# Kernel tuning notes

Hardware: AMD Instinct MI355X
Metric: run time of the kernel (lower is better)

Reference implementation:

```python
import jax, jax.numpy as jnp
import numpy as np

B, T, I, H, O = 128, 512, 512, 2048, 512  # batch, seq_length, input, hidden, output


def setup_inputs() -> dict:
    key = jax.random.key(0)
    ks = jax.random.split(key, 8)
    s_ih = 1.0 / np.sqrt(H)  # torch RNNCell/Linear default init scale 1/sqrt(hidden)
    body = jax.random.normal(ks[0], (B, T - 1, I), dtype=jnp.float32)
    # last timestep row stores the integer pad index (as float), per the module's protocol
    pad = jax.random.randint(ks[1], (B,), 0, T - 2)
    last = jnp.broadcast_to(pad[:, None, None].astype(jnp.float32), (B, 1, I))
    x = jnp.concatenate([body, last], axis=1)  # [B, T, I]
    W_ih = jax.random.uniform(ks[2], (H, I), jnp.float32, -s_ih, s_ih)
    W_hh = jax.random.uniform(ks[3], (H, H), jnp.float32, -s_ih, s_ih)
    b_ih = jax.random.uniform(ks[4], (H,), jnp.float32, -s_ih, s_ih)
    b_hh = jax.random.uniform(ks[5], (H,), jnp.float32, -s_ih, s_ih)
    W_fc = jax.random.uniform(ks[6], (O, H), jnp.float32, -s_ih, s_ih)
    b_fc = jax.random.uniform(ks[7], (O,), jnp.float32, -s_ih, s_ih)
    h0 = jnp.ones((H,), jnp.float32)  # self.h parameter, ones-initialized
    return {"x": x, "h0": h0, "W_ih": W_ih, "b_ih": b_ih, "W_hh": W_hh,
            "b_hh": b_hh, "W_fc": W_fc, "b_fc": b_fc}


def reference(x, h0, W_ih, b_ih, W_hh, b_hh, W_fc, b_fc):
    steps = T - 2  # loop runs over x.shape[2]-1 = (T-1)-1 timesteps
    pad = x[:, -1, 0].astype(jnp.int32)          # [B] pad indices
    xs = jnp.transpose(x[:, :steps, :], (1, 0, 2))  # [steps, B, I]
    h_init = jnp.broadcast_to(h0, (x.shape[0], H))  # self.h * ones([B,1])

    def step(h, xt):
        h = jnp.tanh(xt @ W_ih.T + b_ih + h @ W_hh.T + b_hh)
        return h, h @ W_fc.T + b_fc

    _, outs = jax.lax.scan(step, h_init, xs)     # [steps, B, O]
    # mask selects the single timestep j == pad_len[b]; everything else is zeroed
    mask = (pad[None, :] == jnp.arange(steps)[:, None]).astype(outs.dtype)  # [steps, B]
    return jnp.sum(outs * mask[:, :, None], axis=0)  # [B, O]
```

## Files before the change

kernel.cpp:

```cpp
#include <hip/hip_runtime.h>

#define Bsz 128
#define Tsz 512
#define Isz 512
#define Hsz 2048
#define Osz 512
#define STEPS 510

typedef short short8 __attribute__((ext_vector_type(8)));
typedef float floatx4 __attribute__((ext_vector_type(4)));

__device__ __forceinline__ unsigned short f2bf(float f) {
  unsigned int u = __builtin_bit_cast(unsigned int, f);
  u += 0x7FFFu + ((u >> 16) & 1u);
  return (unsigned short)(u >> 16);
}

template <int AUX>
__device__ __forceinline__ void gload_lds16(const void* g, void* l) {
  __builtin_amdgcn_global_load_lds(
      (const __attribute__((address_space(1))) void*)g,
      (__attribute__((address_space(3))) void*)l, 16, 0, AUX);
}

#define HSTR 2056
#define XSTR 520
#define XBUF (16 * XSTR)

__global__ __launch_bounds__(256, 1)
void rnn_kernel(const float* __restrict__ x, const float* __restrict__ h0v,
                const float* __restrict__ W_ih, const float* __restrict__ b_ih,
                const float* __restrict__ W_hh, const float* __restrict__ b_hh,
                unsigned short* __restrict__ hbuf,
                float* __restrict__ hfinal,
                unsigned int* __restrict__ flags)
{
  __shared__ short h_lds[16 * HSTR];
  __shared__ short x_lds[2 * XBUF];
  __shared__ float red_lds[4 * 16 * 64];
  __shared__ int pad_lds[16];

  const int tid = threadIdx.x;
  const int lane = tid & 63;
  const int wv = tid >> 6;
  const int m16 = lane & 15;
  const int quad = lane >> 4;
  const int rg = blockIdx.x & 7;
  const int cg = blockIdx.x >> 3;
  const int b0 = rg * 16;
  const int c0 = cg * 64;
  const int kq = wv * 512;
  const int kqx = wv * 128;

  short8 wf[16][4];
  short8 wih[4][4];
#pragma unroll
  for (int nt = 0; nt < 4; ++nt) {
    const int wrow = c0 + nt * 16 + m16;
    const float* base = W_hh + (size_t)wrow * Hsz + kq + quad * 8;
#pragma unroll
    for (int kc = 0; kc < 16; ++kc) {
      short8 v;
#pragma unroll
      for (int j = 0; j < 8; ++j) v[j] = (short)f2bf(base[kc * 32 + j]);
      wf[kc][nt] = v;
    }
    const float* basex = W_ih + (size_t)wrow * Isz + kqx + quad * 8;
#pragma unroll
    for (int kc = 0; kc < 4; ++kc) {
      short8 v;
#pragma unroll
      for (int j = 0; j < 8; ++j) v[j] = (short)f2bf(basex[kc * 32 + j]);
      wih[kc][nt] = v;
    }
  }

  const int rrow = tid >> 4;
  const int rcb = (tid & 15) * 4;
  float bias[4];
#pragma unroll
  for (int i = 0; i < 4; ++i) bias[i] = b_ih[c0 + rcb + i] + b_hh[c0 + rcb + i];

  if (tid < 16)
    pad_lds[tid] = (int)x[(size_t)(b0 + tid) * (Tsz * Isz) + (size_t)(Tsz - 1) * Isz];

  for (int k = tid; k < Hsz; k += 256) {
    const short v = (short)f2bf(h0v[k]);
#pragma unroll
    for (int r = 0; r < 16; ++r) h_lds[r * HSTR + k] = v;
  }

  {
    const float* xp = x + (size_t)(b0 + rrow) * (Tsz * Isz);
    short* xb = x_lds + rrow * XSTR;
#pragma unroll
    for (int it = 0; it < 8; ++it) {
      const int i0 = it * 64 + (tid & 15) * 4;
      const float4 v = *reinterpret_cast<const float4*>(xp + i0);
      unsigned long long pk = (unsigned long long)f2bf(v.x) |
                              ((unsigned long long)f2bf(v.y) << 16) |
                              ((unsigned long long)f2bf(v.z) << 32) |
                              ((unsigned long long)f2bf(v.w) << 48);
      *reinterpret_cast<unsigned long long*>(xb + i0) = pk;
    }
  }

  unsigned int* myflag = flags + rg * 32;

  for (int t = 0; t < STEPS; ++t) {
    const bool have_next = (t + 1) < STEPS;

    float4 xv[8];
    if (have_next) {
      const float* xp = x + (size_t)(b0 + rrow) * (Tsz * Isz) + (size_t)(t + 1) * Isz;
#pragma unroll
      for (int it = 0; it < 8; ++it)
        xv[it] = *reinterpret_cast<const float4*>(xp + it * 64 + (tid & 15) * 4);
    }

    if (t > 0) {
      if (tid == 0) {
        const unsigned int target = (unsigned int)(32 * t);
        while (__hip_atomic_load(myflag, __ATOMIC_RELAXED, __HIP_MEMORY_SCOPE_AGENT) < target)
          __builtin_amdgcn_s_sleep(2);
      }
      __syncthreads();
      const unsigned short* hsrc = hbuf + (size_t)(t & 1) * (Bsz * Hsz);
#pragma unroll
      for (int r2 = 0; r2 < 4; ++r2) {
        const int row = wv * 4 + r2;
#pragma unroll
        for (int ch = 0; ch < 4; ++ch) {
          gload_lds16<0x11>(hsrc + (size_t)(b0 + row) * Hsz + ch * 512 + lane * 8,
                            &h_lds[row * HSTR + ch * 512]);
        }
      }
    }

    if (have_next) {
      short* xb = x_lds + ((t + 1) & 1) * XBUF + rrow * XSTR;
#pragma unroll
      for (int it = 0; it < 8; ++it) {
        const int i0 = it * 64 + (tid & 15) * 4;
        unsigned long long pk = (unsigned long long)f2bf(xv[it].x) |
                                ((unsigned long long)f2bf(xv[it].y) << 16) |
                                ((unsigned long long)f2bf(xv[it].z) << 32) |
                                ((unsigned long long)f2bf(xv[it].w) << 48);
        *reinterpret_cast<unsigned long long*>(xb + i0) = pk;
      }
    }

    __syncthreads();

    floatx4 acc[4];
#pragma unroll
    for (int nt = 0; nt < 4; ++nt) {
      floatx4 zero = {0.f, 0.f, 0.f, 0.f};
      acc[nt] = zero;
    }
    {
      const short* xbase = x_lds + (t & 1) * XBUF + m16 * XSTR + kqx + quad * 8;
#pragma unroll
      for (int kc = 0; kc < 4; ++kc) {
        const short8 a = *reinterpret_cast<const short8*>(xbase + kc * 32);
#pragma unroll
        for (int nt = 0; nt < 4; ++nt)
          acc[nt] = __builtin_amdgcn_mfma_f32_16x16x32_bf16(a, wih[kc][nt], acc[nt], 0, 0, 0);
      }
      const short* hbase = h_lds + m16 * HSTR + kq + quad * 8;
#pragma unroll
      for (int kc = 0; kc < 16; ++kc) {
        const short8 a = *reinterpret_cast<const short8*>(hbase + kc * 32);
#pragma unroll
        for (int nt = 0; nt < 4; ++nt)
          acc[nt] = __builtin_amdgcn_mfma_f32_16x16x32_bf16(a, wf[kc][nt], acc[nt], 0, 0, 0);
      }
    }

#pragma unroll
    for (int nt = 0; nt < 4; ++nt)
#pragma unroll
      for (int i = 0; i < 4; ++i)
        red_lds[wv * 1024 + (quad * 4 + i) * 64 + nt * 16 + m16] = acc[nt][i];

    __syncthreads();

    {
      float4 z = {0.f, 0.f, 0.f, 0.f};
#pragma unroll
      for (int ww = 0; ww < 4; ++ww) {
        const float4 p = *reinterpret_cast<const float4*>(&red_lds[ww * 1024 + rrow * 64 + rcb]);
        z.x += p.x; z.y += p.y; z.z += p.z; z.w += p.w;
      }
      const float t0 = tanhf(z.x + bias[0]);
      const float t1 = tanhf(z.y + bias[1]);
      const float t2 = tanhf(z.z + bias[2]);
      const float t3 = tanhf(z.w + bias[3]);
      unsigned long long pk = (unsigned long long)f2bf(t0) |
                              ((unsigned long long)f2bf(t1) << 16) |
                              ((unsigned long long)f2bf(t2) << 32) |
                              ((unsigned long long)f2bf(t3) << 48);
      unsigned short* hd = hbuf + (size_t)((t + 1) & 1) * (Bsz * Hsz) +
                           (size_t)(b0 + rrow) * Hsz + c0 + rcb;
      __hip_atomic_store(reinterpret_cast<unsigned long long*>(hd), pk,
                         __ATOMIC_RELAXED, __HIP_MEMORY_SCOPE_AGENT);
      if (pad_lds[rrow] == t) {
        float4 o;
        o.x = t0; o.y = t1; o.z = t2; o.w = t3;
        *reinterpret_cast<float4*>(&hfinal[(size_t)(b0 + rrow) * Hsz + c0 + rcb]) = o;
      }
    }

    __syncthreads();

    if (have_next && tid == 0) {
      __hip_atomic_fetch_add(myflag, 1u, __ATOMIC_RELAXED, __HIP_MEMORY_SCOPE_AGENT);
    }
  }
}

__global__ __launch_bounds__(64)
void fc_kernel(const float* __restrict__ hfinal, const float* __restrict__ W_fc,
               const float* __restrict__ b_fc, float* __restrict__ out) {
  const int lane = threadIdx.x & 63;
  const int m16 = lane & 15;
  const int quad = lane >> 4;
  const int b0 = (blockIdx.x & 7) * 16;
  const int o0 = (blockIdx.x >> 3) * 16;
  floatx4 acc = {0.f, 0.f, 0.f, 0.f};
  const float* ap = hfinal + (size_t)(b0 + m16) * Hsz + quad * 8;
  const float* bp = W_fc + (size_t)(o0 + m16) * Hsz + quad * 8;
#pragma unroll 4
  for (int kc = 0; kc < 64; ++kc) {
    short8 a, b;
#pragma unroll
    for (int j = 0; j < 8; ++j) a[j] = (short)f2bf(ap[kc * 32 + j]);
#pragma unroll
    for (int j = 0; j < 8; ++j) b[j] = (short)f2bf(bp[kc * 32 + j]);
    acc = __builtin_amdgcn_mfma_f32_16x16x32_bf16(a, b, acc, 0, 0, 0);
  }
  const float bias = b_fc[o0 + m16];
#pragma unroll
  for (int i = 0; i < 4; ++i)
    out[(size_t)(b0 + quad * 4 + i) * Osz + o0 + m16] = acc[i] + bias;
}

__global__ void zero_flags(unsigned int* f) { f[threadIdx.x] = 0u; }

extern "C" void kernel_launch(void* const* d_in, const int* in_sizes, int n_in,
                              void* d_out, int out_size, void* d_ws, size_t ws_size,
                              hipStream_t stream) {
  const float* x = (const float*)d_in[0];
  const float* h0 = (const float*)d_in[1];
  const float* W_ih = (const float*)d_in[2];
  const float* b_ih = (const float*)d_in[3];
  const float* W_hh = (const float*)d_in[4];
  const float* b_hh = (const float*)d_in[5];
  const float* W_fc = (const float*)d_in[6];
  const float* b_fc = (const float*)d_in[7];
  float* out = (float*)d_out;

  char* ws = (char*)d_ws;
  unsigned short* hbuf = (unsigned short*)ws;
  float* hfinal = (float*)(ws + (1u << 20));
  unsigned int* flags = (unsigned int*)(ws + (2u << 20));

  zero_flags<<<1, 256, 0, stream>>>(flags);
  rnn_kernel<<<256, 256, 0, stream>>>(x, h0, W_ih, b_ih, W_hh, b_hh, hbuf, hfinal, flags);
  fc_kernel<<<256, 64, 0, stream>>>(hfinal, W_fc, b_fc, out);
}
```

Before: 2.318 ms.

## Replace per-row-group counter barrier with per-producer flags and per-wave tiled h loads

Each producer block now writes its 16x64 h tile as a contiguous swizzled 1024-element chunk and publishes a per-block step flag. Consumer waves poll only the eight producers covering their K quarter and load each chunk into a private XOR-swizzled LDS region, so waves start as soon as their own inputs arrive instead of waiting on a block-wide barrier. The x tile is loaded straight into MFMA operand registers, which removes the x LDS double buffer and one __syncthreads. The cost is more flag polling per wave, and correctness depends on the swizzle layout and a hand-coded waitcnt matching between producer and consumer.

After: 2.882 ms. +24.3%, slower.

```diff
diff --git a/kernel.cpp b/kernel.cpp
--- a/kernel.cpp
+++ b/kernel.cpp
@@ -22,10 +22,6 @@
       (const __attribute__((address_space(1))) void*)g,
       (__attribute__((address_space(3))) void*)l, 16, 0, AUX);
 }
-
-#define HSTR 2056
-#define XSTR 520
-#define XBUF (16 * XSTR)
 
 __global__ __launch_bounds__(256, 1)
 void rnn_kernel(const float* __restrict__ x, const float* __restrict__ h0v,
@@ -35,9 +31,8 @@
                 float* __restrict__ hfinal,
                 unsigned int* __restrict__ flags)
 {
-  __shared__ short h_lds[16 * HSTR];
-  __shared__ short x_lds[2 * XBUF];
-  __shared__ float red_lds[4 * 16 * 64];
+  __shared__ short h_lds[4 * 8192];
+  __shared__ float red_lds[4 * 1024];
   __shared__ int pad_lds[16];
 
   const int tid = threadIdx.x;
@@ -45,12 +40,14 @@
   const int wv = tid >> 6;
   const int m16 = lane & 15;
   const int quad = lane >> 4;
+  const int m7 = m16 & 7;
   const int rg = blockIdx.x & 7;
   const int cg = blockIdx.x >> 3;
   const int b0 = rg * 16;
   const int c0 = cg * 64;
   const int kq = wv * 512;
   const int kqx = wv * 128;
+  const int wvoff = wv * 8192;
 
   short8 wf[16][4];
   short8 wih[4][4];
@@ -84,73 +81,56 @@
   if (tid < 16)
     pad_lds[tid] = (int)x[(size_t)(b0 + tid) * (Tsz * Isz) + (size_t)(Tsz - 1) * Isz];
 
-  for (int k = tid; k < Hsz; k += 256) {
-    const short v = (short)f2bf(h0v[k]);
-#pragma unroll
-    for (int r = 0; r < 16; ++r) h_lds[r * HSTR + k] = v;
-  }
-
-  {
-    const float* xp = x + (size_t)(b0 + rrow) * (Tsz * Isz);
-    short* xb = x_lds + rrow * XSTR;
-#pragma unroll
-    for (int it = 0; it < 8; ++it) {
-      const int i0 = it * 64 + (tid & 15) * 4;
-      const float4 v = *reinterpret_cast<const float4*>(xp + i0);
-      unsigned long long pk = (unsigned long long)f2bf(v.x) |
-                              ((unsigned long long)f2bf(v.y) << 16) |
-                              ((unsigned long long)f2bf(v.z) << 32) |
-                              ((unsigned long long)f2bf(v.w) << 48);
-      *reinterpret_cast<unsigned long long*>(xb + i0) = pk;
-    }
-  }
-
-  unsigned int* myflag = flags + rg * 32;
+  for (int i = lane; i < 1024; i += 64) {
+    const int c = i >> 7;
+    const int r = (i >> 3) & 15;
+    const int u = i & 7;
+    const int k = kq + c * 64 + u * 8;
+    short8 v;
+#pragma unroll
+    for (int j = 0; j < 8; ++j) v[j] = (short)f2bf(h0v[k + j]);
+    *reinterpret_cast<short8*>(&h_lds[wvoff + c * 1024 + r * 64 + (u ^ (r & 7)) * 8]) = v;
+  }
 
   for (int t = 0; t < STEPS; ++t) {
     const bool have_next = (t + 1) < STEPS;
 
+    const float* xp = x + (size_t)(b0 + m16) * (Tsz * Isz) + (size_t)t * Isz + kqx + quad * 8;
     float4 xv[8];
-    if (have_next) {
-      const float* xp = x + (size_t)(b0 + rrow) * (Tsz * Isz) + (size_t)(t + 1) * Isz;
-#pragma unroll
-      for (int it = 0; it < 8; ++it)
-        xv[it] = *reinterpret_cast<const float4*>(xp + it * 64 + (tid & 15) * 4);
+#pragma unroll
+    for (int kcc = 0; kcc < 4; ++kcc) {
+      xv[2 * kcc] = *reinterpret_cast<const float4*>(xp + kcc * 32);
+      xv[2 * kcc + 1] = *reinterpret_cast<const float4*>(xp + kcc * 32 + 4);
     }
 
     if (t > 0) {
-      if (tid == 0) {
-        const unsigned int target = (unsigned int)(32 * t);
-        while (__hip_atomic_load(myflag, __ATOMIC_RELAXED, __HIP_MEMORY_SCOPE_AGENT) < target)
-          __builtin_amdgcn_s_sleep(2);
-      }
-      __syncthreads();
-      const unsigned short* hsrc = hbuf + (size_t)(t & 1) * (Bsz * Hsz);
-#pragma unroll
-      for (int r2 = 0; r2 < 4; ++r2) {
-        const int row = wv * 4 + r2;
-#pragma unroll
-        for (int ch = 0; ch < 4; ++ch) {
-          gload_lds16<0x11>(hsrc + (size_t)(b0 + row) * Hsz + ch * 512 + lane * 8,
-                            &h_lds[row * HSTR + ch * 512]);
-        }
-      }
-    }
-
-    if (have_next) {
-      short* xb = x_lds + ((t + 1) & 1) * XBUF + rrow * XSTR;
-#pragma unroll
-      for (int it = 0; it < 8; ++it) {
-        const int i0 = it * 64 + (tid & 15) * 4;
-        unsigned long long pk = (unsigned long long)f2bf(xv[it].x) |
-                                ((unsigned long long)f2bf(xv[it].y) << 16) |
-                                ((unsigned long long)f2bf(xv[it].z) << 32) |
-                                ((unsigned long long)f2bf(xv[it].w) << 48);
-        *reinterpret_cast<unsigned long long*>(xb + i0) = pk;
-      }
-    }
-
-    __syncthreads();
+      const unsigned short* hsrcp = hbuf + (size_t)(t & 1) * (Bsz * Hsz);
+#pragma unroll
+      for (int c = 0; c < 8; ++c) {
+        const int cgp = wv * 8 + c;
+        const unsigned int* fp = flags + cgp * 8 + rg;
+        while (__hip_atomic_load(fp, __ATOMIC_RELAXED, __HIP_MEMORY_SCOPE_AGENT) < (unsigned)t)
+          __builtin_amdgcn_s_sleep(1);
+        const unsigned short* src = hsrcp + (size_t)(cgp * 8 + rg) * 1024;
+        gload_lds16<0x11>(src + lane * 8, &h_lds[wvoff + c * 1024]);
+        gload_lds16<0x11>(src + 512 + lane * 8, &h_lds[wvoff + c * 1024 + 512]);
+      }
+    }
+
+    short8 xa[4];
+#pragma unroll
+    for (int kcc = 0; kcc < 4; ++kcc) {
+      short8 a;
+      a[0] = (short)f2bf(xv[2 * kcc].x);
+      a[1] = (short)f2bf(xv[2 * kcc].y);
+      a[2] = (short)f2bf(xv[2 * kcc].z);
+      a[3] = (short)f2bf(xv[2 * kcc].w);
+      a[4] = (short)f2bf(xv[2 * kcc + 1].x);
+      a[5] = (short)f2bf(xv[2 * kcc + 1].y);
+      a[6] = (short)f2bf(xv[2 * kcc + 1].z);
+      a[7] = (short)f2bf(xv[2 * kcc + 1].w);
+      xa[kcc] = a;
+    }
 
     floatx4 acc[4];
 #pragma unroll
@@ -158,22 +138,24 @@
       floatx4 zero = {0.f, 0.f, 0.f, 0.f};
       acc[nt] = zero;
     }
-    {
-      const short* xbase = x_lds + (t & 1) * XBUF + m16 * XSTR + kqx + quad * 8;
-#pragma unroll
-      for (int kc = 0; kc < 4; ++kc) {
-        const short8 a = *reinterpret_cast<const short8*>(xbase + kc * 32);
+#pragma unroll
+    for (int kcc = 0; kcc < 4; ++kcc)
+#pragma unroll
+      for (int nt = 0; nt < 4; ++nt)
+        acc[nt] = __builtin_amdgcn_mfma_f32_16x16x32_bf16(xa[kcc], wih[kcc][nt], acc[nt], 0, 0, 0);
+
+    __builtin_amdgcn_s_waitcnt(0x0F70);
+
+#pragma unroll
+    for (int c = 0; c < 8; ++c) {
+      const int base = wvoff + c * 1024 + m16 * 64;
+#pragma unroll
+      for (int k2 = 0; k2 < 2; ++k2) {
+        const short8 a =
+            *reinterpret_cast<const short8*>(&h_lds[base + ((k2 * 4 + quad) ^ m7) * 8]);
 #pragma unroll
         for (int nt = 0; nt < 4; ++nt)
-          acc[nt] = __builtin_amdgcn_mfma_f32_16x16x32_bf16(a, wih[kc][nt], acc[nt], 0, 0, 0);
-      }
-      const short* hbase = h_lds + m16 * HSTR + kq + quad * 8;
-#pragma unroll
-      for (int kc = 0; kc < 16; ++kc) {
-        const short8 a = *reinterpret_cast<const short8*>(hbase + kc * 32);
-#pragma unroll
-        for (int nt = 0; nt < 4; ++nt)
-          acc[nt] = __builtin_amdgcn_mfma_f32_16x16x32_bf16(a, wf[kc][nt], acc[nt], 0, 0, 0);
+          acc[nt] = __builtin_amdgcn_mfma_f32_16x16x32_bf16(a, wf[c * 2 + k2][nt], acc[nt], 0, 0, 0);
       }
     }
 
@@ -189,7 +171,8 @@
       float4 z = {0.f, 0.f, 0.f, 0.f};
 #pragma unroll
       for (int ww = 0; ww < 4; ++ww) {
-        const float4 p = *reinterpret_cast<const float4*>(&red_lds[ww * 1024 + rrow * 64 + rcb]);
+        const float4 p =
+            *reinterpret_cast<const float4*>(&red_lds[ww * 1024 + rrow * 64 + rcb]);
         z.x += p.x; z.y += p.y; z.z += p.z; z.w += p.w;
       }
       const float t0 = tanhf(z.x + bias[0]);
@@ -200,8 +183,9 @@
                               ((unsigned long long)f2bf(t1) << 16) |
                               ((unsigned long long)f2bf(t2) << 32) |
                               ((unsigned long long)f2bf(t3) << 48);
+      const int toff = rrow * 64 + ((rcb >> 3) ^ (rrow & 7)) * 8 + ((rcb >> 2) & 1) * 4;
       unsigned short* hd = hbuf + (size_t)((t + 1) & 1) * (Bsz * Hsz) +
-                           (size_t)(b0 + rrow) * Hsz + c0 + rcb;
+                           (size_t)(cg * 8 + rg) * 1024 + toff;
       __hip_atomic_store(reinterpret_cast<unsigned long long*>(hd), pk,
                          __ATOMIC_RELAXED, __HIP_MEMORY_SCOPE_AGENT);
       if (pad_lds[rrow] == t) {
@@ -214,7 +198,8 @@
     __syncthreads();
 
     if (have_next && tid == 0) {
-      __hip_atomic_fetch_add(myflag, 1u, __ATOMIC_RELAXED, __HIP_MEMORY_SCOPE_AGENT);
+      __hip_atomic_store(flags + cg * 8 + rg, (unsigned)(t + 1),
+                         __ATOMIC_RELAXED, __HIP_MEMORY_SCOPE_AGENT);
     }
   }
 }
```
